# Optimization experiments

Measured on AMD Instinct MI355X. Metric: run time of the kernel, lower is better.

## Reference

```python
import jax, jax.numpy as jnp
import numpy as np

N, E, IN, H, O, K = 50000, 800000, 256, 128, 32, 5
ALPHA, EPS = 0.1, 1e-5


def setup_inputs() -> dict:
    key = jax.random.key(0)
    ks = jax.random.split(key, 20)
    nrm = lambda k, shape, s=0.02: jax.random.normal(k, shape, dtype=jnp.float32) * s
    H2 = H // 2
    return {
        "x": jax.random.normal(ks[0], (N, IN), dtype=jnp.float32),
        "edge_index": jax.random.randint(ks[1], (2, E), 0, N),
        "edge_weight": jax.random.uniform(ks[2], (E,), dtype=jnp.float32),
        # lin1 + bn1
        "W1": nrm(ks[3], (IN, H)), "b1": jnp.zeros((H,), jnp.float32),
        "g1": jnp.ones((H,), jnp.float32), "be1": jnp.zeros((H,), jnp.float32),
        "m1": nrm(ks[4], (H,), 0.1), "v1": 1.0 + 0.1 * jax.random.uniform(ks[5], (H,), dtype=jnp.float32),
        # lin2 + bn2
        "W2": nrm(ks[6], (H, H)), "b2": jnp.zeros((H,), jnp.float32),
        "g2": jnp.ones((H,), jnp.float32), "be2": jnp.zeros((H,), jnp.float32),
        "m2": nrm(ks[7], (H,), 0.1), "v2": 1.0 + 0.1 * jax.random.uniform(ks[8], (H,), dtype=jnp.float32),
        # attention over hop outputs (K+1)
        "att": jnp.ones((K + 1,), jnp.float32) + nrm(ks[9], (K + 1,), 0.1),
        # head: Linear(H, H//2) + BN + ReLU + Linear(H//2, O)
        "W3": nrm(ks[10], (H, H2)), "b3": jnp.zeros((H2,), jnp.float32),
        "g3": jnp.ones((H2,), jnp.float32), "be3": jnp.zeros((H2,), jnp.float32),
        "m3": nrm(ks[11], (H2,), 0.1), "v3": 1.0 + 0.1 * jax.random.uniform(ks[12], (H2,), dtype=jnp.float32),
        "W4": nrm(ks[13], (H2, O)), "b4": jnp.zeros((O,), jnp.float32),
    }


def _bn(t, g, b, m, v):
    # eval-mode BatchNorm1d using running stats
    return (t - m) * (g / jnp.sqrt(v + EPS)) + b


def reference(x, edge_index, edge_weight, W1, b1, g1, be1, m1, v1,
              W2, b2, g2, be2, m2, v2, att,
              W3, b3, g3, be3, m3, v3, W4, b4):
    n = x.shape[0]
    row, col = edge_index[0], edge_index[1]

    h = jax.nn.relu(_bn(x @ W1 + b1, g1, be1, m1, v1))
    identity = h
    h = jax.nn.relu(_bn(h @ W2 + b2, g2, be2, m2, v2)) + identity

    # weighted edge normalization: out-weight sum per source node, clamped >= 1
    wsum = jnp.maximum(jax.ops.segment_sum(edge_weight, row, num_segments=n), 1.0)
    edge_norm = edge_weight / wsum[row]  # [E]

    def prop(h_in):
        # APPNP-style: K inner iterations blending toward this call's h0
        h0 = h_in
        hk = h_in
        for _ in range(K):
            msg = hk[row] * edge_norm[:, None]          # [E, H] gather + scale
            agg = jax.ops.segment_sum(msg, col, num_segments=n)  # scatter-add
            hk = (1.0 - ALPHA) * agg + ALPHA * h0
        return hk

    xs = [h]
    hc = h
    for _ in range(K):  # outer loop: att has K+1 weights
        hc = prop(hc)
        xs.append(hc)

    stacked = jnp.stack(xs, axis=-1)          # [N, H, K+1]
    w = jax.nn.softmax(att)                   # [K+1]
    fused = jnp.einsum('nhk,k->nh', stacked, w)

    hid = jax.nn.relu(_bn(fused @ W3 + b3, g3, be3, m3, v3))
    return hid @ W4 + b4
```

## Files before the change

kernel.cpp:

```cpp
#include <hip/hip_runtime.h>
#include <cstddef>
#include <cstdint>

namespace {

constexpr int N   = 50000;
constexpr int E   = 800000;
constexpr int IN  = 256;
constexpr int H   = 128;
constexpr int H2v = 64;
constexpr int O   = 32;
constexpr int K   = 5;
constexpr float ALPHA = 0.1f;
constexpr float EPS   = 1e-5f;
constexpr int SCAN_CH = 1024;
constexpr int SCAN_NB = (N + SCAN_CH - 1) / SCAN_CH;
constexpr int NPAD = 50048;
constexpr int NPW  = 4;

typedef __bf16 bf16x8 __attribute__((ext_vector_type(8)));
typedef float  f32x4  __attribute__((ext_vector_type(4)));

__device__ inline uint32_t pack2_bf16(float x, float y) {
  uint32_t ux = __float_as_uint(x);
  uint32_t uy = __float_as_uint(y);
  ux = (ux + 0x7FFFu + ((ux >> 16) & 1u)) >> 16;
  uy = (uy + 0x7FFFu + ((uy >> 16) & 1u)) & 0xFFFF0000u;
  return uy | ux;
}
__device__ inline unsigned short bf16_1(float x) {
  uint32_t u = __float_as_uint(x);
  return (unsigned short)((u + 0x7FFFu + ((u >> 16) & 1u)) >> 16);
}
__device__ inline float bf16_lo(uint32_t v) { return __uint_as_float(v << 16); }
__device__ inline float bf16_hi(uint32_t v) { return __uint_as_float(v & 0xFFFF0000u); }
__device__ inline float bf16_f(unsigned short h) { return __uint_as_float(((uint32_t)h) << 16); }

__global__ void zero2_kernel(int* __restrict__ a, int* __restrict__ b, int n) {
  int i = blockIdx.x * blockDim.x + threadIdx.x;
  if (i < n) { a[i] = 0; b[i] = 0; }
}

__global__ void softmax_att_kernel(const float* __restrict__ att, float* __restrict__ wk) {
  if (threadIdx.x == 0 && blockIdx.x == 0) {
    float mx = att[0];
    for (int i = 1; i < K + 1; ++i) mx = fmaxf(mx, att[i]);
    float ex[K + 1];
    float s = 0.f;
    for (int i = 0; i < K + 1; ++i) { ex[i] = expf(att[i] - mx); s += ex[i]; }
    for (int i = 0; i < K + 1; ++i) wk[i] = ex[i] / s;
  }
}

__global__ void hist_kernel(const int* __restrict__ row, const int* __restrict__ col,
                            const float* __restrict__ ew,
                            int* __restrict__ deg, float* __restrict__ wsum) {
  int i = blockIdx.x * blockDim.x + threadIdx.x;
  if (i < E) {
    atomicAdd(&deg[col[i]], 1);
    atomicAdd(&wsum[row[i]], ew[i]);
  }
}

__global__ __launch_bounds__(256) void scan_local_kernel(const int* __restrict__ deg,
                                                         int* __restrict__ offs,
                                                         int* __restrict__ bsum) {
  __shared__ int sd[256];
  int base = blockIdx.x * SCAN_CH;
  int t = threadIdx.x;
  int v[4];
  int s = 0;
#pragma unroll
  for (int u = 0; u < 4; ++u) {
    int i = base + t * 4 + u;
    v[u] = (i < N) ? deg[i] : 0;
    s += v[u];
  }
  sd[t] = s;
  __syncthreads();
  int val = s;
  for (int off = 1; off < 256; off <<= 1) {
    int x = (t >= off) ? sd[t - off] : 0;
    __syncthreads();
    val += x;
    sd[t] = val;
    __syncthreads();
  }
  int excl = val - s;
#pragma unroll
  for (int u = 0; u < 4; ++u) {
    int i = base + t * 4 + u;
    if (i < N) offs[i] = excl;
    excl += v[u];
  }
  if (t == 255) bsum[blockIdx.x] = val;
}

__global__ void scan_bsum_kernel(int* __restrict__ bsum) {
  if (threadIdx.x == 0 && blockIdx.x == 0) {
    int acc = 0;
    for (int i = 0; i < SCAN_NB; ++i) {
      int v = bsum[i];
      bsum[i] = acc;
      acc += v;
    }
    bsum[SCAN_NB] = acc;
  }
}

__global__ void scan_add_kernel(int* __restrict__ offs, const int* __restrict__ bsum,
                                int* __restrict__ cursor) {
  int i = blockIdx.x * blockDim.x + threadIdx.x;
  if (i < N) {
    int o = offs[i] + bsum[i / SCAN_CH];
    offs[i] = o;
    cursor[i] = o;
  } else if (i <= NPAD) {
    offs[i] = bsum[SCAN_NB];
  }
}

__global__ void fill_kernel(const int* __restrict__ row, const int* __restrict__ col,
                            const float* __restrict__ ew, const float* __restrict__ wsum,
                            int* __restrict__ cursor, uint2* __restrict__ csr) {
  int i = blockIdx.x * blockDim.x + threadIdx.x;
  if (i < E) {
    int d = col[i];
    int p = atomicAdd(&cursor[d], 1);
    int s = row[i];
    float w = ew[i] / fmaxf(wsum[s], 1.0f);
    csr[p] = make_uint2((uint32_t)s, __float_as_uint(w));
  }
}

__global__ void conv_x_kernel(const float* __restrict__ x, unsigned short* __restrict__ xbf) {
  int i = blockIdx.x * blockDim.x + threadIdx.x;
  size_t base = (size_t)i * 8;
  int r = (int)(base / IN);
  uint4 pk = {0, 0, 0, 0};
  if (r < N) {
    float4 a = *(const float4*)&x[base];
    float4 b = *(const float4*)&x[base + 4];
    pk.x = pack2_bf16(a.x, a.y);
    pk.y = pack2_bf16(a.z, a.w);
    pk.z = pack2_bf16(b.x, b.y);
    pk.w = pack2_bf16(b.z, b.w);
  }
  *(uint4*)&xbf[base] = pk;
}

__global__ void conv_wt_kernel(const float* __restrict__ W, unsigned short* __restrict__ Wt,
                               int Kdim) {
  int t = blockIdx.x * blockDim.x + threadIdx.x;
  int k8 = Kdim / 8;
  int n = t / k8;
  int kk = (t % k8) * 8;
  if (n >= H) return;
  float f[8];
#pragma unroll
  for (int j = 0; j < 8; ++j) f[j] = W[(size_t)(kk + j) * H + n];
  uint4 pk;
  pk.x = pack2_bf16(f[0], f[1]);
  pk.y = pack2_bf16(f[2], f[3]);
  pk.z = pack2_bf16(f[4], f[5]);
  pk.w = pack2_bf16(f[6], f[7]);
  *(uint4*)&Wt[(size_t)n * Kdim + kk] = pk;
}

__global__ __launch_bounds__(256) void mlp1_mfma_kernel(
    const unsigned short* __restrict__ xbf, const unsigned short* __restrict__ Wt1,
    const float* __restrict__ b1, const float* __restrict__ g1,
    const float* __restrict__ be1, const float* __restrict__ m1,
    const float* __restrict__ v1, unsigned short* __restrict__ h1bf) {
  int wave = threadIdx.x >> 6;
  int lane = threadIdx.x & 63;
  int m_base = blockIdx.x * 64 + wave * 16;
  int idx16 = lane & 15;
  int quad = lane >> 4;
  bf16x8 afrag[8];
  const unsigned short* xrow = xbf + (size_t)(m_base + idx16) * IN + quad * 8;
#pragma unroll
  for (int k0 = 0; k0 < 8; ++k0) afrag[k0] = *(const bf16x8*)(xrow + k0 * 32);
#pragma unroll
  for (int n0 = 0; n0 < 8; ++n0) {
    f32x4 acc = {0.f, 0.f, 0.f, 0.f};
    const unsigned short* wrow = Wt1 + (size_t)(n0 * 16 + idx16) * IN + quad * 8;
#pragma unroll
    for (int k0 = 0; k0 < 8; ++k0) {
      bf16x8 bfrag = *(const bf16x8*)(wrow + k0 * 32);
      acc = __builtin_amdgcn_mfma_f32_16x16x32_bf16(afrag[k0], bfrag, acc, 0, 0, 0);
    }
    int n = n0 * 16 + idx16;
    float sc = g1[n] * rsqrtf(v1[n] + EPS);
    float ad = b1[n] - m1[n];
    float bb = be1[n];
#pragma unroll
    for (int r = 0; r < 4; ++r) {
      int m = m_base + quad * 4 + r;
      float val = fmaxf((acc[r] + ad) * sc + bb, 0.f);
      h1bf[(size_t)m * H + n] = bf16_1(val);
    }
  }
}

__global__ __launch_bounds__(256) void mlp2_mfma_kernel(
    const unsigned short* __restrict__ h1bf, const unsigned short* __restrict__ Wt2,
    const float* __restrict__ b2, const float* __restrict__ g2,
    const float* __restrict__ be2, const float* __restrict__ m2,
    const float* __restrict__ v2, unsigned short* __restrict__ h0bf,
    float* __restrict__ fused, const float* __restrict__ wk) {
  int wave = threadIdx.x >> 6;
  int lane = threadIdx.x & 63;
  int m_base = blockIdx.x * 64 + wave * 16;
  int idx16 = lane & 15;
  int quad = lane >> 4;
  bf16x8 afrag[4];
  const unsigned short* arow = h1bf + (size_t)(m_base + idx16) * H + quad * 8;
#pragma unroll
  for (int k0 = 0; k0 < 4; ++k0) afrag[k0] = *(const bf16x8*)(arow + k0 * 32);
  float w0 = wk[0];
#pragma unroll
  for (int n0 = 0; n0 < 8; ++n0) {
    f32x4 acc = {0.f, 0.f, 0.f, 0.f};
    const unsigned short* wrow = Wt2 + (size_t)(n0 * 16 + idx16) * H + quad * 8;
#pragma unroll
    for (int k0 = 0; k0 < 4; ++k0) {
      bf16x8 bfrag = *(const bf16x8*)(wrow + k0 * 32);
      acc = __builtin_amdgcn_mfma_f32_16x16x32_bf16(afrag[k0], bfrag, acc, 0, 0, 0);
    }
    int n = n0 * 16 + idx16;
    float sc = g2[n] * rsqrtf(v2[n] + EPS);
    float ad = b2[n] - m2[n];
    float bb = be2[n];
#pragma unroll
    for (int r = 0; r < 4; ++r) {
      int m = m_base + quad * 4 + r;
      if (m < N) {
        float idv = bf16_f(h1bf[(size_t)m * H + n]);
        float val = fmaxf((acc[r] + ad) * sc + bb, 0.f) + idv;
        h0bf[(size_t)m * H + n] = bf16_1(val);
        fused[(size_t)m * H + n] = w0 * val;
      }
    }
  }
}

__global__ __launch_bounds__(256) void prop_kernel(
    const unsigned short* __restrict__ hk, const unsigned short* __restrict__ h0,
    unsigned short* __restrict__ outb,
    const int* __restrict__ offs, const uint2* __restrict__ csr,
    float* __restrict__ fused, const float* __restrict__ wk, int wj) {
  int wave = threadIdx.x >> 6;
  int lane = threadIdx.x & 63;
  int quarter = lane >> 4;
  int colb = (lane & 15) * 8;
  int node0 = (blockIdx.x * 4 + wave) * NPW;
  float wj_w = (wj >= 0) ? wk[wj] : 0.f;
  for (int nn = 0; nn < NPW; ++nn) {
    int node = node0 + nn;
    int beg = offs[node];
    int end = offs[node + 1];
    int deg = end - beg;
    float a[8];
#pragma unroll
    for (int j = 0; j < 8; ++j) a[j] = 0.f;
    int nfull = deg >> 2;
    int qi = 0;
    for (; qi + 4 <= nfull; qi += 4) {
      uint2 ce[4];
      uint4 rv[4];
#pragma unroll
      for (int u = 0; u < 4; ++u) ce[u] = csr[beg + (qi + u) * 4 + quarter];
#pragma unroll
      for (int u = 0; u < 4; ++u) rv[u] = *(const uint4*)&hk[(size_t)ce[u].x * H + colb];
#pragma unroll
      for (int u = 0; u < 4; ++u) {
        float w = __uint_as_float(ce[u].y);
        a[0] += w * bf16_lo(rv[u].x); a[1] += w * bf16_hi(rv[u].x);
        a[2] += w * bf16_lo(rv[u].y); a[3] += w * bf16_hi(rv[u].y);
        a[4] += w * bf16_lo(rv[u].z); a[5] += w * bf16_hi(rv[u].z);
        a[6] += w * bf16_lo(rv[u].w); a[7] += w * bf16_hi(rv[u].w);
      }
    }
    for (; qi < nfull; ++qi) {
      uint2 ce = csr[beg + qi * 4 + quarter];
      uint4 rv = *(const uint4*)&hk[(size_t)ce.x * H + colb];
      float w = __uint_as_float(ce.y);
      a[0] += w * bf16_lo(rv.x); a[1] += w * bf16_hi(rv.x);
      a[2] += w * bf16_lo(rv.y); a[3] += w * bf16_hi(rv.y);
      a[4] += w * bf16_lo(rv.z); a[5] += w * bf16_hi(rv.z);
      a[6] += w * bf16_lo(rv.w); a[7] += w * bf16_hi(rv.w);
    }
    if (deg & 3) {
      int e = beg + nfull * 4 + quarter;
      bool valid = e < end;
      uint2 ce = csr[valid ? e : beg];
      float w = valid ? __uint_as_float(ce.y) : 0.f;
      uint4 rv = *(const uint4*)&hk[(size_t)ce.x * H + colb];
      a[0] += w * bf16_lo(rv.x); a[1] += w * bf16_hi(rv.x);
      a[2] += w * bf16_lo(rv.y); a[3] += w * bf16_hi(rv.y);
      a[4] += w * bf16_lo(rv.z); a[5] += w * bf16_hi(rv.z);
      a[6] += w * bf16_lo(rv.w); a[7] += w * bf16_hi(rv.w);
    }
#pragma unroll
    for (int j = 0; j < 8; ++j) {
      a[j] += __shfl_xor(a[j], 16, 64);
      a[j] += __shfl_xor(a[j], 32, 64);
    }
    size_t idx = (size_t)node * H + colb;
    if (quarter == 0) {
      uint4 hv = *(const uint4*)&h0[idx];
      float v0 = (1.f - ALPHA) * a[0] + ALPHA * bf16_lo(hv.x);
      float v1 = (1.f - ALPHA) * a[1] + ALPHA * bf16_hi(hv.x);
      float v2 = (1.f - ALPHA) * a[2] + ALPHA * bf16_lo(hv.y);
      float v3 = (1.f - ALPHA) * a[3] + ALPHA * bf16_hi(hv.y);
      float v4 = (1.f - ALPHA) * a[4] + ALPHA * bf16_lo(hv.z);
      float v5 = (1.f - ALPHA) * a[5] + ALPHA * bf16_hi(hv.z);
      float v6 = (1.f - ALPHA) * a[6] + ALPHA * bf16_lo(hv.w);
      float v7 = (1.f - ALPHA) * a[7] + ALPHA * bf16_hi(hv.w);
      uint4 pk;
      pk.x = pack2_bf16(v0, v1);
      pk.y = pack2_bf16(v2, v3);
      pk.z = pack2_bf16(v4, v5);
      pk.w = pack2_bf16(v6, v7);
      *(uint4*)&outb[idx] = pk;
    } else if (quarter == 1 && wj >= 0 && node < N) {
      uint4 hv = *(const uint4*)&h0[idx];
      float v0 = (1.f - ALPHA) * a[0] + ALPHA * bf16_lo(hv.x);
      float v1 = (1.f - ALPHA) * a[1] + ALPHA * bf16_hi(hv.x);
      float v2 = (1.f - ALPHA) * a[2] + ALPHA * bf16_lo(hv.y);
      float v3 = (1.f - ALPHA) * a[3] + ALPHA * bf16_hi(hv.y);
      float v4 = (1.f - ALPHA) * a[4] + ALPHA * bf16_lo(hv.z);
      float v5 = (1.f - ALPHA) * a[5] + ALPHA * bf16_hi(hv.z);
      float v6 = (1.f - ALPHA) * a[6] + ALPHA * bf16_lo(hv.w);
      float v7 = (1.f - ALPHA) * a[7] + ALPHA * bf16_hi(hv.w);
      float4 f0 = *(float4*)&fused[idx];
      float4 f1 = *(float4*)&fused[idx + 4];
      f0.x += wj_w * v0; f0.y += wj_w * v1; f0.z += wj_w * v2; f0.w += wj_w * v3;
      f1.x += wj_w * v4; f1.y += wj_w * v5; f1.z += wj_w * v6; f1.w += wj_w * v7;
      *(float4*)&fused[idx] = f0;
      *(float4*)&fused[idx + 4] = f1;
    }
  }
}

__global__ __launch_bounds__(64) void head_kernel(
    const float* __restrict__ fused, const float* __restrict__ W3,
    const float* __restrict__ b3, const float* __restrict__ g3,
    const float* __restrict__ be3, const float* __restrict__ m3,
    const float* __restrict__ v3, const float* __restrict__ W4,
    const float* __restrict__ b4, float* __restrict__ out) {
  __shared__ float fl[16][H];
  __shared__ float hl[16][H2v];
  int node0 = blockIdx.x * 16;
  int t = threadIdx.x;
  for (int idx = t * 4; idx < 16 * H; idx += 64 * 4) {
    int r = idx >> 7, c = idx & (H - 1);
    *(float4*)&fl[r][c] = *(const float4*)&fused[(size_t)(node0 + r) * H + c];
  }
  __syncthreads();
  {
    int ng = t >> 4;
    int c0 = (t & 15) * 4;
    float acc[4][4];
#pragma unroll
    for (int a = 0; a < 4; ++a)
#pragma unroll
      for (int b = 0; b < 4; ++b) acc[a][b] = 0.f;
    for (int k = 0; k < H; k += 4) {
      float4 xv[4];
#pragma unroll
      for (int a = 0; a < 4; ++a) xv[a] = *(const float4*)&fl[ng * 4 + a][k];
      float4 wv[4];
#pragma unroll
      for (int j = 0; j < 4; ++j) wv[j] = *(const float4*)&W3[(size_t)(k + j) * H2v + c0];
#pragma unroll
      for (int a = 0; a < 4; ++a) {
        float xa0 = xv[a].x, xa1 = xv[a].y, xa2 = xv[a].z, xa3 = xv[a].w;
        acc[a][0] += xa0 * wv[0].x + xa1 * wv[1].x + xa2 * wv[2].x + xa3 * wv[3].x;
        acc[a][1] += xa0 * wv[0].y + xa1 * wv[1].y + xa2 * wv[2].y + xa3 * wv[3].y;
        acc[a][2] += xa0 * wv[0].z + xa1 * wv[1].z + xa2 * wv[2].z + xa3 * wv[3].z;
        acc[a][3] += xa0 * wv[0].w + xa1 * wv[1].w + xa2 * wv[2].w + xa3 * wv[3].w;
      }
    }
    float sc[4], ad[4], bb[4];
#pragma unroll
    for (int b = 0; b < 4; ++b) {
      int c = c0 + b;
      sc[b] = g3[c] * rsqrtf(v3[c] + EPS);
      ad[b] = b3[c] - m3[c];
      bb[b] = be3[c];
    }
#pragma unroll
    for (int a = 0; a < 4; ++a)
#pragma unroll
      for (int b = 0; b < 4; ++b)
        hl[ng * 4 + a][c0 + b] = fmaxf((acc[a][b] + ad[b]) * sc[b] + bb[b], 0.f);
  }
  __syncthreads();
  {
    int co = t & 31;
    int nh = t >> 5;
    float bias = b4[co];
#pragma unroll
    for (int a = 0; a < 8; ++a) {
      int nloc = nh * 8 + a;
      float accf = bias;
      for (int k = 0; k < H2v; k += 4) {
        float4 hv = *(const float4*)&hl[nloc][k];
        accf += hv.x * W4[(size_t)(k + 0) * O + co];
        accf += hv.y * W4[(size_t)(k + 1) * O + co];
        accf += hv.z * W4[(size_t)(k + 2) * O + co];
        accf += hv.w * W4[(size_t)(k + 3) * O + co];
      }
      out[(size_t)(node0 + nloc) * O + co] = accf;
    }
  }
}

}

extern "C" void kernel_launch(void* const* d_in, const int* in_sizes, int n_in,
                              void* d_out, int out_size, void* d_ws, size_t ws_size,
                              hipStream_t stream) {
  const float* x   = (const float*)d_in[0];
  const int*   ei  = (const int*)d_in[1];
  const float* ew  = (const float*)d_in[2];
  const float* W1  = (const float*)d_in[3];
  const float* b1  = (const float*)d_in[4];
  const float* g1  = (const float*)d_in[5];
  const float* be1 = (const float*)d_in[6];
  const float* m1  = (const float*)d_in[7];
  const float* v1  = (const float*)d_in[8];
  const float* W2  = (const float*)d_in[9];
  const float* b2  = (const float*)d_in[10];
  const float* g2  = (const float*)d_in[11];
  const float* be2 = (const float*)d_in[12];
  const float* m2  = (const float*)d_in[13];
  const float* v2  = (const float*)d_in[14];
  const float* att = (const float*)d_in[15];
  const float* W3  = (const float*)d_in[16];
  const float* b3  = (const float*)d_in[17];
  const float* g3  = (const float*)d_in[18];
  const float* be3 = (const float*)d_in[19];
  const float* m3  = (const float*)d_in[20];
  const float* v3  = (const float*)d_in[21];
  const float* W4  = (const float*)d_in[22];
  const float* b4  = (const float*)d_in[23];
  const int* row = ei;
  const int* col = ei + E;
  float* out = (float*)d_out;

  char* p = (char*)d_ws;
  auto carve = [&](size_t bytes) -> void* {
    void* q = (void*)p;
    p += (bytes + 255) & ~(size_t)255;
    return q;
  };
  int*   deg     = (int*)carve((size_t)N * 4);
  float* wsum    = (float*)carve((size_t)N * 4);
  int*   offs    = (int*)carve((size_t)(NPAD + 1) * 4);
  int*   cursor  = (int*)carve((size_t)N * 4);
  int*   bsum    = (int*)carve((size_t)(SCAN_NB + 1) * 4);
  uint2* csr     = (uint2*)carve((size_t)E * 8);
  float* wk      = (float*)carve(64);
  unsigned short* xbf  = (unsigned short*)carve((size_t)NPAD * IN * 2);
  unsigned short* Wt1  = (unsigned short*)carve((size_t)H * IN * 2);
  unsigned short* Wt2  = (unsigned short*)carve((size_t)H * H * 2);
  unsigned short* h1bf = (unsigned short*)carve((size_t)NPAD * H * 2);
  unsigned short* bf0  = (unsigned short*)carve((size_t)NPAD * H * 2);
  unsigned short* bfA  = (unsigned short*)carve((size_t)NPAD * H * 2);
  unsigned short* bfB  = (unsigned short*)carve((size_t)NPAD * H * 2);
  float* fused   = (float*)carve((size_t)N * H * 4);

  const int tb = 256;
  zero2_kernel<<<(N + tb - 1) / tb, tb, 0, stream>>>(deg, (int*)wsum, N);
  softmax_att_kernel<<<1, 64, 0, stream>>>(att, wk);
  hist_kernel<<<(E + tb - 1) / tb, tb, 0, stream>>>(row, col, ew, deg, wsum);
  scan_local_kernel<<<SCAN_NB, 256, 0, stream>>>(deg, offs, bsum);
  scan_bsum_kernel<<<1, 64, 0, stream>>>(bsum);
  scan_add_kernel<<<(NPAD + 1 + tb - 1) / tb, tb, 0, stream>>>(offs, bsum, cursor);
  fill_kernel<<<(E + tb - 1) / tb, tb, 0, stream>>>(row, col, ew, wsum, cursor, csr);

  conv_x_kernel<<<(NPAD * IN / 8 + tb - 1) / tb, tb, 0, stream>>>(x, xbf);
  conv_wt_kernel<<<(H * (IN / 8) + tb - 1) / tb, tb, 0, stream>>>(W1, Wt1, IN);
  conv_wt_kernel<<<(H * (H / 8) + tb - 1) / tb, tb, 0, stream>>>(W2, Wt2, H);

  mlp1_mfma_kernel<<<NPAD / 64, 256, 0, stream>>>(xbf, Wt1, b1, g1, be1, m1, v1, h1bf);
  mlp2_mfma_kernel<<<NPAD / 64, 256, 0, stream>>>(h1bf, Wt2, b2, g2, be2, m2, v2,
                                                  bf0, fused, wk);

  unsigned short* h0 = bf0;
  unsigned short* pa = bfA;
  unsigned short* pb = bfB;
  const int prop_blocks = NPAD / (4 * NPW);
  for (int j = 1; j <= K; ++j) {
    const unsigned short* src = h0;
    unsigned short* dst = pa;
    for (int i = 0; i < K; ++i) {
      int wj = (i == K - 1) ? j : -1;
      prop_kernel<<<prop_blocks, 256, 0, stream>>>(src, h0, dst, offs, csr, fused, wk, wj);
      if (i < K - 1) {
        src = dst;
        dst = (dst == pa) ? pb : pa;
      }
    }
    unsigned short* oldh0 = h0;
    h0 = pa;
    pa = pb;
    pb = oldh0;
  }

  head_kernel<<<N / 16, 64, 0, stream>>>(fused, W3, b3, g3, be3, m3, v3, W4, b4, out);
}
```

Baseline: 1.269 ms.

## Privatize histogram atomics into 8 copies and fuse x bf16 conversion into mlp1

Degree and weight-sum histograms and the CSR fill cursors are spread across 8 per-block-group copies. A reduce kernel then combines them and builds per-copy cursor bases, which is meant to cut atomic contention on hot nodes. Separately, the standalone x-to-bf16 conversion kernel is removed and mlp1 reads fp32 x and packs it to bf16 in registers. That saves a full write and reread of the converted x buffer. The privatization adds an extra kernel and more zeroing and reduction traffic.

Measured after the change: 1.250 ms. No clear change (-1.5%).

```diff
diff --git a/kernel.cpp b/kernel.cpp
--- a/kernel.cpp
+++ b/kernel.cpp
@@ -17,6 +17,7 @@
 constexpr int SCAN_NB = (N + SCAN_CH - 1) / SCAN_CH;
 constexpr int NPAD = 50048;
 constexpr int NPW  = 4;
+constexpr int NC   = 8;
 
 typedef __bf16 bf16x8 __attribute__((ext_vector_type(8)));
 typedef float  f32x4  __attribute__((ext_vector_type(4)));
@@ -36,9 +37,9 @@
 __device__ inline float bf16_hi(uint32_t v) { return __uint_as_float(v & 0xFFFF0000u); }
 __device__ inline float bf16_f(unsigned short h) { return __uint_as_float(((uint32_t)h) << 16); }
 
-__global__ void zero2_kernel(int* __restrict__ a, int* __restrict__ b, int n) {
+__global__ void zero_kernel(uint32_t* __restrict__ p, int n) {
   int i = blockIdx.x * blockDim.x + threadIdx.x;
-  if (i < n) { a[i] = 0; b[i] = 0; }
+  if (i < n) p[i] = 0;
 }
 
 __global__ void softmax_att_kernel(const float* __restrict__ att, float* __restrict__ wk) {
@@ -54,12 +55,31 @@
 
 __global__ void hist_kernel(const int* __restrict__ row, const int* __restrict__ col,
                             const float* __restrict__ ew,
-                            int* __restrict__ deg, float* __restrict__ wsum) {
+                            int* __restrict__ deg8, float* __restrict__ wsum8) {
   int i = blockIdx.x * blockDim.x + threadIdx.x;
+  int c = blockIdx.x & (NC - 1);
   if (i < E) {
-    atomicAdd(&deg[col[i]], 1);
-    atomicAdd(&wsum[row[i]], ew[i]);
-  }
+    atomicAdd(&deg8[c * N + col[i]], 1);
+    atomicAdd(&wsum8[c * N + row[i]], ew[i]);
+  }
+}
+
+__global__ void reduce8_kernel(int* __restrict__ deg8, float* __restrict__ wsum8,
+                               int* __restrict__ deg, float* __restrict__ wsum) {
+  int i = blockIdx.x * blockDim.x + threadIdx.x;
+  if (i >= N) return;
+  int tot = 0;
+#pragma unroll
+  for (int x = 0; x < NC; ++x) {
+    int v = deg8[x * N + i];
+    deg8[x * N + i] = tot;
+    tot += v;
+  }
+  deg[i] = tot;
+  float ws = 0.f;
+#pragma unroll
+  for (int x = 0; x < NC; ++x) ws += wsum8[x * N + i];
+  wsum[i] = ws;
 }
 
 __global__ __launch_bounds__(256) void scan_local_kernel(const int* __restrict__ deg,
@@ -109,12 +129,13 @@
 }
 
 __global__ void scan_add_kernel(int* __restrict__ offs, const int* __restrict__ bsum,
-                                int* __restrict__ cursor) {
+                                int* __restrict__ deg8) {
   int i = blockIdx.x * blockDim.x + threadIdx.x;
   if (i < N) {
     int o = offs[i] + bsum[i / SCAN_CH];
     offs[i] = o;
-    cursor[i] = o;
+#pragma unroll
+    for (int x = 0; x < NC; ++x) deg8[x * N + i] += o;
   } else if (i <= NPAD) {
     offs[i] = bsum[SCAN_NB];
   }
@@ -122,31 +143,16 @@
 
 __global__ void fill_kernel(const int* __restrict__ row, const int* __restrict__ col,
                             const float* __restrict__ ew, const float* __restrict__ wsum,
-                            int* __restrict__ cursor, uint2* __restrict__ csr) {
+                            int* __restrict__ cursor8, uint2* __restrict__ csr) {
   int i = blockIdx.x * blockDim.x + threadIdx.x;
+  int c = blockIdx.x & (NC - 1);
   if (i < E) {
     int d = col[i];
-    int p = atomicAdd(&cursor[d], 1);
+    int p = atomicAdd(&cursor8[c * N + d], 1);
     int s = row[i];
     float w = ew[i] / fmaxf(wsum[s], 1.0f);
     csr[p] = make_uint2((uint32_t)s, __float_as_uint(w));
   }
-}
-
-__global__ void conv_x_kernel(const float* __restrict__ x, unsigned short* __restrict__ xbf) {
-  int i = blockIdx.x * blockDim.x + threadIdx.x;
-  size_t base = (size_t)i * 8;
-  int r = (int)(base / IN);
-  uint4 pk = {0, 0, 0, 0};
-  if (r < N) {
-    float4 a = *(const float4*)&x[base];
-    float4 b = *(const float4*)&x[base + 4];
-    pk.x = pack2_bf16(a.x, a.y);
-    pk.y = pack2_bf16(a.z, a.w);
-    pk.z = pack2_bf16(b.x, b.y);
-    pk.w = pack2_bf16(b.z, b.w);
-  }
-  *(uint4*)&xbf[base] = pk;
 }
 
 __global__ void conv_wt_kernel(const float* __restrict__ W, unsigned short* __restrict__ Wt,
@@ -168,7 +174,7 @@
 }
 
 __global__ __launch_bounds__(256) void mlp1_mfma_kernel(
-    const unsigned short* __restrict__ xbf, const unsigned short* __restrict__ Wt1,
+    const float* __restrict__ x, const unsigned short* __restrict__ Wt1,
     const float* __restrict__ b1, const float* __restrict__ g1,
     const float* __restrict__ be1, const float* __restrict__ m1,
     const float* __restrict__ v1, unsigned short* __restrict__ h1bf) {
@@ -177,10 +183,26 @@
   int m_base = blockIdx.x * 64 + wave * 16;
   int idx16 = lane & 15;
   int quad = lane >> 4;
+  int m = m_base + idx16;
   bf16x8 afrag[8];
-  const unsigned short* xrow = xbf + (size_t)(m_base + idx16) * IN + quad * 8;
-#pragma unroll
-  for (int k0 = 0; k0 < 8; ++k0) afrag[k0] = *(const bf16x8*)(xrow + k0 * 32);
+  if (m < N) {
+    const float* xrow = x + (size_t)m * IN + quad * 8;
+#pragma unroll
+    for (int k0 = 0; k0 < 8; ++k0) {
+      float4 a = *(const float4*)(xrow + k0 * 32);
+      float4 b = *(const float4*)(xrow + k0 * 32 + 4);
+      uint4 pk;
+      pk.x = pack2_bf16(a.x, a.y);
+      pk.y = pack2_bf16(a.z, a.w);
+      pk.z = pack2_bf16(b.x, b.y);
+      pk.w = pack2_bf16(b.z, b.w);
+      afrag[k0] = *(bf16x8*)&pk;
+    }
+  } else {
+    uint4 z = {0, 0, 0, 0};
+#pragma unroll
+    for (int k0 = 0; k0 < 8; ++k0) afrag[k0] = *(bf16x8*)&z;
+  }
 #pragma unroll
   for (int n0 = 0; n0 < 8; ++n0) {
     f32x4 acc = {0.f, 0.f, 0.f, 0.f};
@@ -196,9 +218,9 @@
     float bb = be1[n];
 #pragma unroll
     for (int r = 0; r < 4; ++r) {
-      int m = m_base + quad * 4 + r;
+      int mm = m_base + quad * 4 + r;
       float val = fmaxf((acc[r] + ad) * sc + bb, 0.f);
-      h1bf[(size_t)m * H + n] = bf16_1(val);
+      h1bf[(size_t)mm * H + n] = bf16_1(val);
     }
   }
 }
@@ -457,14 +479,14 @@
     p += (bytes + 255) & ~(size_t)255;
     return q;
   };
+  int*   deg8    = (int*)carve((size_t)NC * N * 4);
+  float* wsum8   = (float*)carve((size_t)NC * N * 4);
   int*   deg     = (int*)carve((size_t)N * 4);
   float* wsum    = (float*)carve((size_t)N * 4);
   int*   offs    = (int*)carve((size_t)(NPAD + 1) * 4);
-  int*   cursor  = (int*)carve((size_t)N * 4);
   int*   bsum    = (int*)carve((size_t)(SCAN_NB + 1) * 4);
   uint2* csr     = (uint2*)carve((size_t)E * 8);
   float* wk      = (float*)carve(64);
-  unsigned short* xbf  = (unsigned short*)carve((size_t)NPAD * IN * 2);
   unsigned short* Wt1  = (unsigned short*)carve((size_t)H * IN * 2);
   unsigned short* Wt2  = (unsigned short*)carve((size_t)H * H * 2);
   unsigned short* h1bf = (unsigned short*)carve((size_t)NPAD * H * 2);
@@ -474,19 +496,19 @@
   float* fused   = (float*)carve((size_t)N * H * 4);
 
   const int tb = 256;
-  zero2_kernel<<<(N + tb - 1) / tb, tb, 0, stream>>>(deg, (int*)wsum, N);
+  zero_kernel<<<(2 * NC * N + tb - 1) / tb, tb, 0, stream>>>((uint32_t*)deg8, 2 * NC * N);
   softmax_att_kernel<<<1, 64, 0, stream>>>(att, wk);
-  hist_kernel<<<(E + tb - 1) / tb, tb, 0, stream>>>(row, col, ew, deg, wsum);
+  hist_kernel<<<(E + tb - 1) / tb, tb, 0, stream>>>(row, col, ew, deg8, wsum8);
+  reduce8_kernel<<<(N + tb - 1) / tb, tb, 0, stream>>>(deg8, wsum8, deg, wsum);
   scan_local_kernel<<<SCAN_NB, 256, 0, stream>>>(deg, offs, bsum);
   scan_bsum_kernel<<<1, 64, 0, stream>>>(bsum);
-  scan_add_kernel<<<(NPAD + 1 + tb - 1) / tb, tb, 0, stream>>>(offs, bsum, cursor);
-  fill_kernel<<<(E + tb - 1) / tb, tb, 0, stream>>>(row, col, ew, wsum, cursor, csr);
-
-  conv_x_kernel<<<(NPAD * IN / 8 + tb - 1) / tb, tb, 0, stream>>>(x, xbf);
+  scan_add_kernel<<<(NPAD + 1 + tb - 1) / tb, tb, 0, stream>>>(offs, bsum, deg8);
+  fill_kernel<<<(E + tb - 1) / tb, tb, 0, stream>>>(row, col, ew, wsum, deg8, csr);
+
   conv_wt_kernel<<<(H * (IN / 8) + tb - 1) / tb, tb, 0, stream>>>(W1, Wt1, IN);
   conv_wt_kernel<<<(H * (H / 8) + tb - 1) / tb, tb, 0, stream>>>(W2, Wt2, H);
 
-  mlp1_mfma_kernel<<<NPAD / 64, 256, 0, stream>>>(xbf, Wt1, b1, g1, be1, m1, v1, h1bf);
+  mlp1_mfma_kernel<<<NPAD / 64, 256, 0, stream>>>(x, Wt1, b1, g1, be1, m1, v1, h1bf);
   mlp2_mfma_kernel<<<NPAD / 64, 256, 0, stream>>>(h1bf, Wt2, b2, g2, be2, m2, v2,
                                                   bf0, fused, wk);
 
```
